# Performance work log

Hardware: AMD Instinct MI355X
Metric: run time of the kernel (lower is better)

## Reference

```python
import jax, jax.numpy as jnp
import numpy as np

WINDOW = 7
SIGMA = 1.5
C1 = 0.01 ** 2
C2 = 0.03 ** 2


def gaussian_kernel():
    coords = jnp.arange(WINDOW, dtype=jnp.float32) - WINDOW // 2
    g = jnp.exp(-coords ** 2 / (2 * SIGMA ** 2))
    k = g[None, :] * g[:, None]
    k = k / k.sum()
    return k[None, None, :, :]  # [O=1, I=1, 7, 7]


def _conv(img, k):
    # img: [B,1,H,W], k: [1,1,7,7]; SAME padding matches torch pad=window//2
    return jax.lax.conv_general_dilated(
        img, k, window_strides=(1, 1), padding='SAME',
        dimension_numbers=('NCHW', 'OIHW', 'NCHW'))


def setup_inputs() -> dict:
    key = jax.random.key(0)
    kx, ky = jax.random.split(key)
    x = jax.random.uniform(kx, (32, 1, 512, 512), dtype=jnp.float32)
    y = jax.random.uniform(ky, (32, 1, 512, 512), dtype=jnp.float32)
    return {"x": x, "y": y, "kernel": gaussian_kernel()}


def reference(x, y, kernel):
    x = x.astype(jnp.float32)
    y = y.astype(jnp.float32)
    mu_x = _conv(x, kernel)
    mu_y = _conv(y, kernel)
    s_xx = _conv(x * x, kernel) - mu_x * mu_x
    s_yy = _conv(y * y, kernel) - mu_y * mu_y
    s_xy = _conv(x * y, kernel) - mu_x * mu_y
    num = (2 * mu_x * mu_y + C1) * (2 * s_xy + C2)
    den = (mu_x ** 2 + mu_y ** 2 + C1) * (s_xx + s_yy + C2)
    return (num / den).mean()
```

## Files before the change

kernel.cpp:

```cpp
#include <hip/hip_runtime.h>

#define IMG_H 512
#define IMG_W 512
#define BATCH 32
#define TW 256
#define TH 16
#define NROWS (TH + 6)
#define NBLK (2 * 32 * 32)

__global__ __launch_bounds__(256) void ssim_main(
    const float* __restrict__ X, const float* __restrict__ Y,
    const float* __restrict__ K, float* __restrict__ partials) {
  __shared__ float2 sbuf[2][264];
  __shared__ float wsum[4];

  const int t = threadIdx.x;
  const int x0 = blockIdx.x * TW;
  const int y0 = blockIdx.y * TH;
  const size_t img = (size_t)IMG_H * IMG_W;
  const float* Xb = X + blockIdx.z * img;
  const float* Yb = Y + blockIdx.z * img;

  float w[7];
  {
    float rs = 0.f;
#pragma unroll
    for (int j = 0; j < 7; ++j) { w[j] = K[3 * 7 + j]; rs += w[j]; }
    const float inv = 1.f / rs;
#pragma unroll
    for (int j = 0; j < 7; ++j) w[j] *= inv;
  }

  const int g1 = x0 - 3 + t;
  const bool ok1 = (unsigned)g1 < (unsigned)IMG_W;
  const int g2 = g1 + TW;
  const bool ok2 = (t < 6) && ((unsigned)g2 < (unsigned)IMG_W);

  float acc[7][5];
#pragma unroll
  for (int s = 0; s < 7; ++s)
#pragma unroll
    for (int c = 0; c < 5; ++c) acc[s][c] = 0.f;
  float tsum = 0.f;

  float pxa, pya, pxb, pyb;
  auto load_row = [&](int r) {
    const int gy = y0 - 3 + r;
    pxa = 0.f; pya = 0.f; pxb = 0.f; pyb = 0.f;
    if ((unsigned)gy < (unsigned)IMG_H) {
      const float* xrow = Xb + (size_t)gy * IMG_W;
      const float* yrow = Yb + (size_t)gy * IMG_W;
      if (ok1) { pxa = xrow[g1]; pya = yrow[g1]; }
      if (ok2) { pxb = xrow[g2]; pyb = yrow[g2]; }
    }
  };

  load_row(0);

#pragma unroll
  for (int r = 0; r < NROWS; ++r) {
    const int buf = r & 1;

    sbuf[buf][t] = make_float2(pxa, pya);
    if (t < 6) sbuf[buf][TW + t] = make_float2(pxb, pyb);

    if (r + 1 < NROWS) load_row(r + 1);

    __syncthreads();

    float hx = 0.f, hy = 0.f, hxx = 0.f, hyy = 0.f, hxy = 0.f;
#pragma unroll
    for (int k = 0; k < 7; ++k) {
      const float2 p = sbuf[buf][t + k];
      const float wx = w[k] * p.x;
      const float wy = w[k] * p.y;
      hx  = fmaf(w[k], p.x, hx);
      hy  = fmaf(w[k], p.y, hy);
      hxx = fmaf(wx, p.x, hxx);
      hyy = fmaf(wy, p.y, hyy);
      hxy = fmaf(wx, p.y, hxy);
    }

#pragma unroll
    for (int tt = 0; tt < 7; ++tt) {
      const int o = r - tt;
      if (o >= 0 && o < TH) {
        const int slot = o % 7;
        const float wt = w[tt];
        acc[slot][0] = fmaf(wt, hx,  acc[slot][0]);
        acc[slot][1] = fmaf(wt, hy,  acc[slot][1]);
        acc[slot][2] = fmaf(wt, hxx, acc[slot][2]);
        acc[slot][3] = fmaf(wt, hyy, acc[slot][3]);
        acc[slot][4] = fmaf(wt, hxy, acc[slot][4]);
      }
    }

    if (r >= 6 && r - 6 < TH) {
      const int slot = (r - 6) % 7;
      const float mu_x = acc[slot][0];
      const float mu_y = acc[slot][1];
      const float mx2 = mu_x * mu_x;
      const float my2 = mu_y * mu_y;
      const float mxy = mu_x * mu_y;
      const float sxx = acc[slot][2] - mx2;
      const float syy = acc[slot][3] - my2;
      const float sxy = acc[slot][4] - mxy;
      const float num = (2.f * mxy + 1e-4f) * (2.f * sxy + 9e-4f);
      const float den = (mx2 + my2 + 1e-4f) * (sxx + syy + 9e-4f);
      tsum += num * __builtin_amdgcn_rcpf(den);
#pragma unroll
      for (int c = 0; c < 5; ++c) acc[slot][c] = 0.f;
    }
  }

#pragma unroll
  for (int off = 32; off > 0; off >>= 1) tsum += __shfl_down(tsum, off);
  if ((t & 63) == 0) wsum[t >> 6] = tsum;
  __syncthreads();
  if (t == 0) {
    const int bid = blockIdx.x + 2 * (blockIdx.y + 32 * blockIdx.z);
    partials[bid] = wsum[0] + wsum[1] + wsum[2] + wsum[3];
  }
}

__global__ __launch_bounds__(256) void ssim_reduce(
    const float* __restrict__ partials, float* __restrict__ out) {
  __shared__ double wsum[4];
  const int t = threadIdx.x;
  double s = 0.0;
#pragma unroll
  for (int i = 0; i < NBLK / 256; ++i) s += (double)partials[t + 256 * i];
#pragma unroll
  for (int off = 32; off > 0; off >>= 1) s += __shfl_down(s, off);
  if ((t & 63) == 0) wsum[t >> 6] = s;
  __syncthreads();
  if (t == 0)
    out[0] = (float)((wsum[0] + wsum[1] + wsum[2] + wsum[3]) *
                     (1.0 / (double)((size_t)BATCH * IMG_H * IMG_W)));
}

extern "C" void kernel_launch(void* const* d_in, const int* in_sizes, int n_in,
                              void* d_out, int out_size, void* d_ws, size_t ws_size,
                              hipStream_t stream) {
  const float* X = (const float*)d_in[0];
  const float* Y = (const float*)d_in[1];
  const float* K = (const float*)d_in[2];
  float* out = (float*)d_out;
  float* partials = (float*)d_ws;

  dim3 grid(IMG_W / TW, IMG_H / TH, BATCH);
  hipLaunchKernelGGL(ssim_main, grid, dim3(256), 0, stream, X, Y, K, partials);
  hipLaunchKernelGGL(ssim_reduce, dim3(1), dim3(256), 0, stream, partials, out);
}
```

Before: 114.4 us.

## Replace shared-memory row staging with per-thread direct global loads of 7 taps

Removes the LDS row buffer and the per-row __syncthreads. Each thread now loads its 7 horizontal neighbours for x and y straight from global memory, using clamped indices and zeroed weights at the edges. Out-of-range rows are clamped and masked by multiplying by zero. This drops the barrier and LDS traffic but issues about 7x more global load instructions per row and relies on L1/L2 cache to absorb the redundancy. It also raises register pressure.

Measured after the change: 170.1 us. 48.7% more time.

```diff
diff --git a/kernel.cpp b/kernel.cpp
--- a/kernel.cpp
+++ b/kernel.cpp
@@ -11,7 +11,6 @@
 __global__ __launch_bounds__(256) void ssim_main(
     const float* __restrict__ X, const float* __restrict__ Y,
     const float* __restrict__ K, float* __restrict__ partials) {
-  __shared__ float2 sbuf[2][264];
   __shared__ float wsum[4];
 
   const int t = threadIdx.x;
@@ -31,10 +30,15 @@
     for (int j = 0; j < 7; ++j) w[j] *= inv;
   }
 
-  const int g1 = x0 - 3 + t;
-  const bool ok1 = (unsigned)g1 < (unsigned)IMG_W;
-  const int g2 = g1 + TW;
-  const bool ok2 = (t < 6) && ((unsigned)g2 < (unsigned)IMG_W);
+  const int col = x0 + t;
+  int idx[7];
+  float wk[7];
+#pragma unroll
+  for (int k = 0; k < 7; ++k) {
+    const int c = col - 3 + k;
+    idx[k] = min(max(c, 0), IMG_W - 1);
+    wk[k] = ((unsigned)c < (unsigned)IMG_W) ? w[k] : 0.f;
+  }
 
   float acc[7][5];
 #pragma unroll
@@ -43,43 +47,43 @@
     for (int c = 0; c < 5; ++c) acc[s][c] = 0.f;
   float tsum = 0.f;
 
-  float pxa, pya, pxb, pyb;
-  auto load_row = [&](int r) {
+  float xv[2][7], yv[2][7];
+  auto load_row = [&](int r, int b) {
     const int gy = y0 - 3 + r;
-    pxa = 0.f; pya = 0.f; pxb = 0.f; pyb = 0.f;
-    if ((unsigned)gy < (unsigned)IMG_H) {
-      const float* xrow = Xb + (size_t)gy * IMG_W;
-      const float* yrow = Yb + (size_t)gy * IMG_W;
-      if (ok1) { pxa = xrow[g1]; pya = yrow[g1]; }
-      if (ok2) { pxb = xrow[g2]; pyb = yrow[g2]; }
+    const int gyc = min(max(gy, 0), IMG_H - 1);
+    const float* xrow = Xb + (size_t)gyc * IMG_W;
+    const float* yrow = Yb + (size_t)gyc * IMG_W;
+#pragma unroll
+    for (int k = 0; k < 7; ++k) {
+      xv[b][k] = xrow[idx[k]];
+      yv[b][k] = yrow[idx[k]];
     }
   };
 
-  load_row(0);
+  load_row(0, 0);
 
 #pragma unroll
   for (int r = 0; r < NROWS; ++r) {
-    const int buf = r & 1;
-
-    sbuf[buf][t] = make_float2(pxa, pya);
-    if (t < 6) sbuf[buf][TW + t] = make_float2(pxb, pyb);
-
-    if (r + 1 < NROWS) load_row(r + 1);
-
-    __syncthreads();
+    const int b = r & 1;
+    if (r + 1 < NROWS) load_row(r + 1, b ^ 1);
 
     float hx = 0.f, hy = 0.f, hxx = 0.f, hyy = 0.f, hxy = 0.f;
 #pragma unroll
     for (int k = 0; k < 7; ++k) {
-      const float2 p = sbuf[buf][t + k];
-      const float wx = w[k] * p.x;
-      const float wy = w[k] * p.y;
-      hx  = fmaf(w[k], p.x, hx);
-      hy  = fmaf(w[k], p.y, hy);
-      hxx = fmaf(wx, p.x, hxx);
-      hyy = fmaf(wy, p.y, hyy);
-      hxy = fmaf(wx, p.y, hxy);
+      const float xvk = xv[b][k];
+      const float yvk = yv[b][k];
+      const float wx = wk[k] * xvk;
+      const float wy = wk[k] * yvk;
+      hx  = fmaf(wk[k], xvk, hx);
+      hy  = fmaf(wk[k], yvk, hy);
+      hxx = fmaf(wx, xvk, hxx);
+      hyy = fmaf(wy, yvk, hyy);
+      hxy = fmaf(wx, yvk, hxy);
     }
+
+    const int gy = y0 - 3 + r;
+    const float rm = ((unsigned)gy < (unsigned)IMG_H) ? 1.f : 0.f;
+    hx *= rm; hy *= rm; hxx *= rm; hyy *= rm; hxy *= rm;
 
 #pragma unroll
     for (int tt = 0; tt < 7; ++tt) {
@@ -95,7 +99,7 @@
       }
     }
 
-    if (r >= 6 && r - 6 < TH) {
+    if (r >= 6) {
       const int slot = (r - 6) % 7;
       const float mu_x = acc[slot][0];
       const float mu_y = acc[slot][1];
```
